# Performance work log

Measured on AMD Instinct MI355X. Metric: run time of the kernel, lower is better.

## Reference

```python
import jax, jax.numpy as jnp
import numpy as np

N = 1024
D_IN = 512
D = 128
E = 8192


def setup_inputs() -> dict:
    key = jax.random.key(0)
    ks = jax.random.split(key, 7)
    return {
        "inputs": jax.random.normal(ks[0], (N, D_IN), dtype=jnp.float32),
        "adj": jax.random.uniform(ks[1], (N, N), dtype=jnp.float32),
        "weight": jax.random.normal(ks[2], (D_IN, D), dtype=jnp.float32) * 0.05,
        "weight_two": jax.random.normal(ks[3], (2 * D, D), dtype=jnp.float32) * 0.05,
        "weight_three": jax.random.normal(ks[4], (2 * D, 1), dtype=jnp.float32) * 0.05,
        "train_edges": jax.random.randint(ks[5], (E, 2), 0, N, dtype=jnp.int64 if jax.config.jax_enable_x64 else jnp.int32),
        "train_false_edges": jax.random.randint(ks[6], (E, 2), 0, N, dtype=jnp.int64 if jax.config.jax_enable_x64 else jnp.int32),
    }


def reference(inputs, adj, weight, weight_two, weight_three, train_edges, train_false_edges):
    # encoder: x = X W ; z = A x   (single GCN-style layer, no bias)
    x = inputs @ weight          # (N, D)
    z = adj @ x                  # (N, D)
    n, d = z.shape

    # all-pairs features: pair (i, j) -> [z_i ; z_j]  (torch repeat/reshape semantics)
    z1 = jnp.broadcast_to(z[:, None, :], (n, n, d))   # z1[i,j] = z[i]
    z2 = jnp.broadcast_to(z[None, :, :], (n, n, d))   # z2[i,j] = z[j]

    z_pair = jax.nn.relu(jnp.concatenate([z1, z2], axis=-1))   # (N, N, 2D)
    z_pair = jnp.einsum('ijk,kl->ijl', z_pair, weight_two)     # (N, N, D)
    z_em = z1 * z2                                             # (N, N, D)

    score = jnp.einsum('ijk,kl->ijl', jnp.concatenate([z_pair, z_em], axis=-1), weight_three)
    return jax.nn.sigmoid(score[..., 0])  # (N, N)
```

## Files before the change

### kernel.cpp

```cpp
#include <hip/hip_runtime.h>
#include <math.h>

#define NN 1024
#define DIN 512
#define DD 128

static constexpr long X_OFF = 0;
static constexpr long Z_OFF = X_OFF + (long)NN * DD;
static constexpr long U_OFF = Z_OFF + (long)NN * DD;

__global__ __launch_bounds__(512) void k1_x_zeroz_u(
    const float* __restrict__ inputs, const float* __restrict__ W,
    const float* __restrict__ W2, const float* __restrict__ w3,
    float* __restrict__ x, float* __restrict__ z, float* __restrict__ u) {
  const int t = threadIdx.x;
  const int bx = blockIdx.x;
  const int by = blockIdx.y;
  const int blk = bx * 4 + by;

  if (t < 256) {
    float4 zz; zz.x = 0.f; zz.y = 0.f; zz.z = 0.f; zz.w = 0.f;
    ((float4*)z)[(long)blk * 256 + t] = zz;
  }

  const int tx = t & 31;
  const int ty = t >> 5;
  const int c  = by * 32 + tx;
  const int r0 = bx * 32 + ty;
  const float* A0 = inputs + (long)r0 * DIN;
  const float* A1 = inputs + (long)(r0 + 16) * DIN;
  float acc0 = 0.f, acc1 = 0.f;
#pragma unroll 4
  for (int k = 0; k < DIN; k += 4) {
    const float4 a0 = *(const float4*)&A0[k];
    const float4 a1 = *(const float4*)&A1[k];
    const float b0 = W[(long)k * DD + c];
    const float b1 = W[(long)(k + 1) * DD + c];
    const float b2 = W[(long)(k + 2) * DD + c];
    const float b3 = W[(long)(k + 3) * DD + c];
    acc0 += a0.x * b0 + a0.y * b1 + a0.z * b2 + a0.w * b3;
    acc1 += a1.x * b0 + a1.y * b1 + a1.z * b2 + a1.w * b3;
  }
  x[(long)r0 * DD + c] = acc0;
  x[(long)(r0 + 16) * DD + c] = acc1;

  if (blk < 8 && t < 256) {
    const int row = blk * 32 + (t >> 3);
    const int l8 = t & 7;
    float s = 0.f;
#pragma unroll
    for (int i = 0; i < 16; ++i) {
      const int l = l8 + 8 * i;
      s += W2[(long)row * DD + l] * w3[l];
    }
#pragma unroll
    for (int off = 4; off > 0; off >>= 1) s += __shfl_down(s, off, 8);
    if (l8 == 0) u[row] = s;
  }
}

__global__ __launch_bounds__(256) void k2_z_atomic(
    const float* __restrict__ adj, const float* __restrict__ x,
    float* __restrict__ z) {
  const int t = threadIdx.x;
  const int tx = t & 31;
  const int ty = t >> 5;
  const int row0 = blockIdx.x * 32;
  const int k0 = blockIdx.y * 128;

  float acc[4][4] = {};

  for (int k = k0; k < k0 + 128; k += 4) {
    float bv[4][4];
#pragma unroll
    for (int kk = 0; kk < 4; ++kk) {
      const float* Brow = &x[(long)(k + kk) * DD + tx];
#pragma unroll
      for (int mc = 0; mc < 4; ++mc) bv[kk][mc] = Brow[32 * mc];
    }
#pragma unroll
    for (int mr = 0; mr < 4; ++mr) {
      const int r = row0 + ty + 8 * mr;
      const float4 av = *(const float4*)&adj[(long)r * NN + k];
      const float ar[4] = {av.x, av.y, av.z, av.w};
#pragma unroll
      for (int kk = 0; kk < 4; ++kk)
#pragma unroll
        for (int mc = 0; mc < 4; ++mc) acc[mr][mc] += ar[kk] * bv[kk][mc];
    }
  }

#pragma unroll
  for (int mr = 0; mr < 4; ++mr) {
    const int r = row0 + ty + 8 * mr;
#pragma unroll
    for (int mc = 0; mc < 4; ++mc)
      atomicAdd(&z[(long)r * DD + tx + 32 * mc], acc[mr][mc]);
  }
}

__global__ __launch_bounds__(256) void k3_decode(
    const float* __restrict__ z, const float* __restrict__ w3,
    const float* __restrict__ u, float* __restrict__ out) {
  __shared__ float zwl[64 * DD];
  __shared__ float a_loc[64];
  __shared__ float b_loc[64];
  const int t = threadIdx.x;
  const int i0 = blockIdx.y * 64;
  const int j0 = blockIdx.x * 64;

#pragma unroll
  for (int s = 0; s < 8; ++s) {
    const int q = s * 256 + t;
    const int r = q >> 5;
    const int k4 = (q & 31) << 2;
    const float4 u0 = *(const float4*)&u[k4];
    const float4 u1 = *(const float4*)&u[DD + k4];
    const float4 v = *(const float4*)&z[(long)(i0 + r) * DD + k4];
    float pa = fmaxf(v.x, 0.f) * u0.x + fmaxf(v.y, 0.f) * u0.y +
               fmaxf(v.z, 0.f) * u0.z + fmaxf(v.w, 0.f) * u0.w;
    float4 w = *(const float4*)&z[(long)(j0 + r) * DD + k4];
    float pb = fmaxf(w.x, 0.f) * u1.x + fmaxf(w.y, 0.f) * u1.y +
               fmaxf(w.z, 0.f) * u1.z + fmaxf(w.w, 0.f) * u1.w;
    const float4 cc = *(const float4*)&w3[DD + k4];
    w.x *= cc.x; w.y *= cc.y; w.z *= cc.z; w.w *= cc.w;
    *(float4*)&zwl[r * DD + (k4 ^ ((r & 7) << 2))] = w;
#pragma unroll
    for (int off = 16; off > 0; off >>= 1) {
      pa += __shfl_down(pa, off, 32);
      pb += __shfl_down(pb, off, 32);
    }
    if ((t & 31) == 0) { a_loc[r] = pa; b_loc[r] = pb; }
  }
  __syncthreads();

  const int tx = t & 15;
  const int ty = t >> 4;
  float acc[4][4] = {};
  for (int k4 = 0; k4 < DD; k4 += 4) {
    float4 ar[4], bc[4];
#pragma unroll
    for (int m = 0; m < 4; ++m)
      ar[m] = *(const float4*)&z[(long)(i0 + ty + 16 * m) * DD + k4];
#pragma unroll
    for (int m = 0; m < 4; ++m) {
      const int C = tx + 16 * m;
      bc[m] = *(const float4*)&zwl[C * DD + (k4 ^ ((C & 7) << 2))];
    }
#pragma unroll
    for (int mr = 0; mr < 4; ++mr)
#pragma unroll
      for (int mc = 0; mc < 4; ++mc)
        acc[mr][mc] += ar[mr].x * bc[mc].x + ar[mr].y * bc[mc].y +
                       ar[mr].z * bc[mc].z + ar[mr].w * bc[mc].w;
  }

#pragma unroll
  for (int mr = 0; mr < 4; ++mr) {
    const int i = i0 + ty + 16 * mr;
    const float ai = a_loc[ty + 16 * mr];
#pragma unroll
    for (int mc = 0; mc < 4; ++mc) {
      const int j = j0 + tx + 16 * mc;
      const float s = ai + b_loc[tx + 16 * mc] + acc[mr][mc];
      out[(long)i * NN + j] = 1.0f / (1.0f + __expf(-s));
    }
  }
}

extern "C" void kernel_launch(void* const* d_in, const int* in_sizes, int n_in,
                              void* d_out, int out_size, void* d_ws, size_t ws_size,
                              hipStream_t stream) {
  (void)in_sizes; (void)n_in; (void)out_size; (void)ws_size;
  const float* inputs = (const float*)d_in[0];
  const float* adj    = (const float*)d_in[1];
  const float* weight = (const float*)d_in[2];
  const float* W2     = (const float*)d_in[3];
  const float* w3     = (const float*)d_in[4];
  float* out = (float*)d_out;

  float* ws = (float*)d_ws;
  float* x = ws + X_OFF;
  float* z = ws + Z_OFF;
  float* u = ws + U_OFF;

  k1_x_zeroz_u<<<dim3(32, 4), 512, 0, stream>>>(inputs, weight, W2, w3, x, z, u);
  k2_z_atomic<<<dim3(32, 8), 256, 0, stream>>>(adj, x, z);
  k3_decode<<<dim3(16, 16), 256, 0, stream>>>(z, w3, u, out);
}
```

Measured before the change: 126.8 us.

## Replace atomic split-K reduction with partial buffers and a finalize kernel

Result: no change. 125.1 us (-1.4%).

```diff
diff --git a/kernel.cpp b/kernel.cpp
--- a/kernel.cpp
+++ b/kernel.cpp
@@ -5,24 +5,21 @@
 #define DIN 512
 #define DD 128
 
-static constexpr long X_OFF = 0;
-static constexpr long Z_OFF = X_OFF + (long)NN * DD;
-static constexpr long U_OFF = Z_OFF + (long)NN * DD;
-
-__global__ __launch_bounds__(512) void k1_x_zeroz_u(
+static constexpr long S = (long)NN * DD;
+static constexpr long ZP_OFF = 0;
+static constexpr long X_OFF  = ZP_OFF + 8 * S;
+static constexpr long Z_OFF  = X_OFF + S;
+static constexpr long U_OFF  = Z_OFF + S;
+static constexpr long A_OFF  = U_OFF + 256;
+static constexpr long B_OFF  = A_OFF + NN;
+
+__global__ __launch_bounds__(512) void k1_x_u(
     const float* __restrict__ inputs, const float* __restrict__ W,
     const float* __restrict__ W2, const float* __restrict__ w3,
-    float* __restrict__ x, float* __restrict__ z, float* __restrict__ u) {
+    float* __restrict__ x, float* __restrict__ u) {
   const int t = threadIdx.x;
   const int bx = blockIdx.x;
   const int by = blockIdx.y;
-  const int blk = bx * 4 + by;
-
-  if (t < 256) {
-    float4 zz; zz.x = 0.f; zz.y = 0.f; zz.z = 0.f; zz.w = 0.f;
-    ((float4*)z)[(long)blk * 256 + t] = zz;
-  }
-
   const int tx = t & 31;
   const int ty = t >> 5;
   const int c  = by * 32 + tx;
@@ -44,6 +41,7 @@
   x[(long)r0 * DD + c] = acc0;
   x[(long)(r0 + 16) * DD + c] = acc1;
 
+  const int blk = bx * 4 + by;
   if (blk < 8 && t < 256) {
     const int row = blk * 32 + (t >> 3);
     const int l8 = t & 7;
@@ -59,9 +57,9 @@
   }
 }
 
-__global__ __launch_bounds__(256) void k2_z_atomic(
+__global__ __launch_bounds__(256) void k2_zp(
     const float* __restrict__ adj, const float* __restrict__ x,
-    float* __restrict__ z) {
+    float* __restrict__ zp) {
   const int t = threadIdx.x;
   const int tx = t & 31;
   const int ty = t >> 5;
@@ -90,21 +88,49 @@
     }
   }
 
+  float* Cs = zp + (long)blockIdx.y * S;
 #pragma unroll
   for (int mr = 0; mr < 4; ++mr) {
     const int r = row0 + ty + 8 * mr;
 #pragma unroll
     for (int mc = 0; mc < 4; ++mc)
-      atomicAdd(&z[(long)r * DD + tx + 32 * mc], acc[mr][mc]);
-  }
-}
-
-__global__ __launch_bounds__(256) void k3_decode(
+      Cs[(long)r * DD + tx + 32 * mc] = acc[mr][mc];
+  }
+}
+
+__global__ __launch_bounds__(128) void k3_finalize(
+    const float* __restrict__ zp, float* __restrict__ z,
+    const float* __restrict__ u, float* __restrict__ a, float* __restrict__ b) {
+  __shared__ float red[2][2];
+  const int i = blockIdx.x;
+  const int c = threadIdx.x;
+  float s = 0.f;
+#pragma unroll
+  for (int p = 0; p < 8; ++p) s += zp[p * S + (long)i * DD + c];
+  z[(long)i * DD + c] = s;
+
+  const float r = s > 0.f ? s : 0.f;
+  float pa = r * u[c];
+  float pb = r * u[DD + c];
+#pragma unroll
+  for (int off = 32; off > 0; off >>= 1) {
+    pa += __shfl_down(pa, off);
+    pb += __shfl_down(pb, off);
+  }
+  const int w = c >> 6;
+  if ((c & 63) == 0) { red[w][0] = pa; red[w][1] = pb; }
+  __syncthreads();
+  if (c == 0) {
+    a[i] = red[0][0] + red[1][0];
+    b[i] = red[0][1] + red[1][1];
+  }
+}
+
+__global__ __launch_bounds__(256) void k4_decode(
     const float* __restrict__ z, const float* __restrict__ w3,
-    const float* __restrict__ u, float* __restrict__ out) {
+    const float* __restrict__ a, const float* __restrict__ b,
+    float* __restrict__ out) {
   __shared__ float zwl[64 * DD];
-  __shared__ float a_loc[64];
-  __shared__ float b_loc[64];
   const int t = threadIdx.x;
   const int i0 = blockIdx.y * 64;
   const int j0 = blockIdx.x * 64;
@@ -114,23 +140,10 @@
     const int q = s * 256 + t;
     const int r = q >> 5;
     const int k4 = (q & 31) << 2;
-    const float4 u0 = *(const float4*)&u[k4];
-    const float4 u1 = *(const float4*)&u[DD + k4];
-    const float4 v = *(const float4*)&z[(long)(i0 + r) * DD + k4];
-    float pa = fmaxf(v.x, 0.f) * u0.x + fmaxf(v.y, 0.f) * u0.y +
-               fmaxf(v.z, 0.f) * u0.z + fmaxf(v.w, 0.f) * u0.w;
     float4 w = *(const float4*)&z[(long)(j0 + r) * DD + k4];
-    float pb = fmaxf(w.x, 0.f) * u1.x + fmaxf(w.y, 0.f) * u1.y +
-               fmaxf(w.z, 0.f) * u1.z + fmaxf(w.w, 0.f) * u1.w;
     const float4 cc = *(const float4*)&w3[DD + k4];
     w.x *= cc.x; w.y *= cc.y; w.z *= cc.z; w.w *= cc.w;
     *(float4*)&zwl[r * DD + (k4 ^ ((r & 7) << 2))] = w;
-#pragma unroll
-    for (int off = 16; off > 0; off >>= 1) {
-      pa += __shfl_down(pa, off, 32);
-      pb += __shfl_down(pb, off, 32);
-    }
-    if ((t & 31) == 0) { a_loc[r] = pa; b_loc[r] = pb; }
   }
   __syncthreads();
 
@@ -158,12 +171,12 @@
 #pragma unroll
   for (int mr = 0; mr < 4; ++mr) {
     const int i = i0 + ty + 16 * mr;
-    const float ai = a_loc[ty + 16 * mr];
+    const float ai = a[i];
 #pragma unroll
     for (int mc = 0; mc < 4; ++mc) {
       const int j = j0 + tx + 16 * mc;
-      const float s = ai + b_loc[tx + 16 * mc] + acc[mr][mc];
-      out[(long)i * NN + j] = 1.0f / (1.0f + __expf(-s));
+      const float sc = ai + b[j] + acc[mr][mc];
+      out[(long)i * NN + j] = 1.0f / (1.0f + __expf(-sc));
     }
   }
 }
@@ -180,11 +193,15 @@
   float* out = (float*)d_out;
 
   float* ws = (float*)d_ws;
-  float* x = ws + X_OFF;
-  float* z = ws + Z_OFF;
-  float* u = ws + U_OFF;
-
-  k1_x_zeroz_u<<<dim3(32, 4), 512, 0, stream>>>(inputs, weight, W2, w3, x, z, u);
-  k2_z_atomic<<<dim3(32, 8), 256, 0, stream>>>(adj, x, z);
-  k3_decode<<<dim3(16, 16), 256, 0, stream>>>(z, w3, u, out);
-}
+  float* zp = ws + ZP_OFF;
+  float* x  = ws + X_OFF;
+  float* z  = ws + Z_OFF;
+  float* u  = ws + U_OFF;
+  float* a  = ws + A_OFF;
+  float* b  = ws + B_OFF;
+
+  k1_x_u<<<dim3(32, 4), 512, 0, stream>>>(inputs, weight, W2, w3, x, u);
+  k2_zp<<<dim3(32, 8), 256, 0, stream>>>(adj, x, zp);
+  k3_finalize<<<1024, 128, 0, stream>>>(zp, z, u, a, b);
+  k4_decode<<<dim3(16, 16), 256, 0, stream>>>(z, w3, a, b, out);
+}
```
